# Performance work log

Measured on AMD Instinct MI355X. Metric: run time of the kernel, lower is better.

Reference implementation:

```python
import math
import jax
import jax.numpy as jnp
import numpy as np

B, N = 64, 64
R = N * (N - 1)
DIST_THRESH = 0.35


def _pair_indices(n):
    # edge e = i*(n-1) + j - (j > i): row-major over i, ascending j skipping j == i
    ii = np.repeat(np.arange(n), n - 1)
    jm = np.tile(np.arange(n), (n, 1))
    jj = jm[~np.eye(n, dtype=bool)].reshape(-1)
    return ii, jj


def _rot_basis(a):
    # a: [..., 1] angle -> [..., 2, 2] rotation basis rows [cos,sin],[cos(a+pi/2),sin(a+pi/2)]
    first = jnp.concatenate([jnp.cos(a), jnp.sin(a)], axis=-1)
    second = jnp.concatenate([jnp.cos(a + math.pi / 2), jnp.sin(a + math.pi / 2)], axis=-1)
    return jnp.stack([first, second], axis=-2)


def setup_inputs() -> dict:
    ks = jax.random.split(jax.random.key(0), 8)
    nrm = lambda k, shape, s=1.0: (jax.random.normal(k, shape) * s).astype(jnp.float32)
    return dict(
        objects_state=jax.random.uniform(ks[0], (B, N, 8), dtype=jnp.float32),
        objects_shape=nrm(ks[1], (B, N, 10)),
        relation_info=nrm(ks[2], (B, R, 3)),
        s_mean=jnp.zeros((8,), jnp.float32), s_std=jnp.ones((8,), jnp.float32),
        sh_mean=jnp.zeros((10,), jnp.float32), sh_std=jnp.ones((10,), jnp.float32),
        v_mean=jnp.zeros((3,), jnp.float32), v_std=jnp.ones((3,), jnp.float32),
        W1=nrm(ks[3], (32, 256), 32 ** -0.5), b1=jnp.zeros((256,), jnp.float32),
        W2=nrm(ks[4], (256, 128), 256 ** -0.5), b2=jnp.zeros((128,), jnp.float32),
        W3=nrm(ks[5], (141, 256), 141 ** -0.5), b3=jnp.zeros((256,), jnp.float32),
        W4=nrm(ks[6], (256, 3), 256 ** -0.5), b4=jnp.zeros((3,), jnp.float32),
    )


def reference(objects_state, objects_shape, relation_info, s_mean, s_std, sh_mean, sh_std,
              v_mean, v_std, W1, b1, W2, b2, W3, b3, W4, b4):
    n = objects_state.shape[1]
    ii, jj = _pair_indices(n)

    # ---- pre_proces: distance-threshold edge build into dense one-hot matrices ----
    pos = objects_state[:, :, 0:2]
    dist = jnp.sqrt(jnp.sum((pos[:, :, None, :] - pos[:, None, :, :]) ** 2, axis=-1))
    # torch: where(dist<0.35, dist, 0).nonzero() -> keeps dist<0.35 AND dist != 0 (drops self-edges)
    mask = ((dist < DIST_THRESH) & (dist != 0.0)).astype(jnp.float32)
    mask_flat = mask[:, ii, jj]  # [B, R]
    eye = jnp.eye(n, dtype=jnp.float32)
    receiver_relations = mask_flat[:, :, None] * eye[ii][None]  # [B, R, N]
    sender_relations = mask_flat[:, :, None] * eye[jj][None]    # [B, R, N]

    data_state = (objects_state - s_mean) / s_std
    data_shape = (objects_shape - sh_mean) / sh_std

    senders_state = jnp.einsum('brn,bnd->brd', sender_relations, data_state)
    receivers_state = jnp.einsum('brn,bnd->brd', receiver_relations, data_state)
    senders_shape = jnp.einsum('brn,bnd->brd', sender_relations, data_shape)
    receivers_shape = jnp.einsum('brn,bnd->brd', receiver_relations, data_shape)

    basis = _rot_basis(receivers_state[:, :, 2:3])  # [B, R, 2, 2]
    diff_state = senders_state - receivers_state
    temp = jnp.stack([diff_state[:, :, 0:2], diff_state[:, :, 3:5], senders_state[:, :, 6:8]], axis=-1)  # [B,R,2,3]
    tfed = jnp.einsum('brij,brjk->brik', basis, temp)  # [B,R,2,3]
    angle_diff = diff_state[:, :, 2:3]
    diff_feat = jnp.concatenate([
        tfed[:, :, :, 0], tfed[:, :, :, 1], tfed[:, :, :, 2],
        jnp.sin(2 * angle_diff), jnp.cos(2 * angle_diff),
        diff_state[:, :, 5:6],
    ], axis=-1)  # [B, R, 9]
    rel_data = jnp.concatenate([relation_info, diff_feat, receivers_shape, senders_shape], axis=-1)  # [B,R,32]

    obj_basis = _rot_basis(data_state[:, :, 2:3])  # [B, N, 2, 2]
    obj_vel_tfed = jnp.einsum('bnij,bnj->bni', obj_basis, data_state[:, :, 3:5])
    obj_data = jnp.concatenate([obj_vel_tfed, data_state[:, :, 5:6], data_shape], axis=-1)  # [B,N,13]

    # ---- interaction-network Net ----
    effects = jax.nn.relu(rel_data @ W1 + b1) @ W2 + b2  # [B, R, 128]
    agg = jnp.einsum('brn,bre->bne', receiver_relations, effects)  # [B, N, 128]
    out_vel = jax.nn.relu(jnp.concatenate([obj_data, agg], axis=-1) @ W3 + b3) @ W4 + b4  # [B,N,3]

    # ---- post_proces ----
    angles = objects_state[:, 1:, 2:3]
    pred = out_vel[:, 1:, :] * v_std + v_mean  # inv_transform_vel
    basis_back = _rot_basis(-angles)
    vel_back = jnp.einsum('bnij,bnj->bni', basis_back, pred[:, :, :2])
    x_dot = jnp.concatenate([vel_back, pred[:, :, 2:]], axis=-1)  # [B, N-1, 3]

    tp = np.eye(6, dtype=np.float32)
    tp[3:, 3:] = 0.0
    tq = np.zeros((3, 6), dtype=np.float32)
    for i in range(3):
        tq[i, i] = 1.0
        tq[i, 3 + i] = 1.0
    x_next = objects_state[:, 1:, :6] @ jnp.asarray(tp) + x_dot @ jnp.asarray(tq)
    return x_next  # [B, N-1, 6]
```

## Files before the change

kernel.cpp:

```cpp
#include <hip/hip_runtime.h>
#include <math.h>

#define BB 64
#define NN 64
#define NM1 63
#define RR (NN*(NN-1))

typedef short bf16x8 __attribute__((ext_vector_type(8)));
typedef float f32x4 __attribute__((ext_vector_type(4)));
union U4 { uint4 u; bf16x8 b; };

__device__ inline unsigned int f2bf(float f) {
    unsigned int u = __float_as_uint(f);
    return (u + 0x7FFFu + ((u >> 16) & 1u)) >> 16;
}
__device__ inline unsigned int pack2(float a, float b) {
    return f2bf(a) | (f2bf(b) << 16);
}

__global__ __launch_bounds__(512, 4) void fused_kernel(
    const float* __restrict__ objects_state,
    const float* __restrict__ objects_shape,
    const float* __restrict__ relation_info,
    const float* __restrict__ s_mean, const float* __restrict__ s_std,
    const float* __restrict__ sh_mean, const float* __restrict__ sh_std,
    const float* __restrict__ v_mean, const float* __restrict__ v_std,
    const float* __restrict__ W1, const float* __restrict__ b1,
    const float* __restrict__ W2, const float* __restrict__ b2,
    const float* __restrict__ W3, const float* __restrict__ b3,
    const float* __restrict__ W4, const float* __restrict__ b4,
    float* __restrict__ out)
{
    __shared__ __align__(16) float P[64][28];
    __shared__ __align__(16) unsigned int relb_w[8*64*16];
    __shared__ __align__(16) unsigned short s_h[16*264];
    __shared__ __align__(16) unsigned short s_q[16*168];
    __shared__ int   s_cntg[8];
    __shared__ float s_red[8][16][3];
    __shared__ float s_outv[16][3];

    const int b  = blockIdx.x >> 3;
    const int nb = (blockIdx.x & 7) * 8;
    const int t  = threadIdx.x;
    const int wv = t >> 6, lane = t & 63, col16 = lane & 15, quad = lane >> 4;

    float w1v[16], b10, b11;
    {
        const int cA = wv*32 + col16, cB = cA + 16;
        #pragma unroll
        for (int j = 0; j < 8; ++j) {
            const int k = quad*8 + j;
            const int orig = k < 12 ? k : (k < 22 ? k+10 : k-10);
            w1v[j]   = W1[orig*256 + cA];
            w1v[8+j] = W1[orig*256 + cB];
        }
        b10 = b1[cA]; b11 = b1[cB];
    }

    float ri0 = 0.f, ri1 = 0.f, ri2 = 0.f;
    if (t < 504) {
        const float* rp = relation_info + ((size_t)b*RR + nb*NM1 + t)*3;
        ri0 = rp[0]; ri1 = rp[1]; ri2 = rp[2];
    }

    float e_vs0=0.f,e_vs1=0.f,e_vs2=0.f,e_vm0=0.f,e_vm1=0.f,e_vm2=0.f,e_b4=0.f;
    if (t < 48) {
        e_vs0 = v_std[0]; e_vs1 = v_std[1]; e_vs2 = v_std[2];
        e_vm0 = v_mean[0]; e_vm1 = v_mean[1]; e_vm2 = v_mean[2];
        e_b4  = b4[t % 3];
    }

    {
        uint4 z = make_uint4(0,0,0,0);
        uint4* relb4 = (uint4*)relb_w;
        #pragma unroll
        for (int r = 0; r < 4; ++r) relb4[r*512 + t] = z;
        if (t < 336) ((uint4*)s_q)[t] = z;
        if (t < 8) s_cntg[t] = 0;
        if (t < 64) {
            const int n = b*64 + t;
            const float4* sp4 = (const float4*)(objects_state + (size_t)n*8);
            const float4 sA = sp4[0], sB = sp4[1];
            float st[8] = {sA.x, sA.y, sA.z, sA.w, sB.x, sB.y, sB.z, sB.w};
            const float2* hp2 = (const float2*)(objects_shape + (size_t)n*10);
            float sh[10];
            #pragma unroll
            for (int c = 0; c < 5; ++c) {
                const float2 v = hp2[c];
                sh[c*2] = v.x; sh[c*2+1] = v.y;
            }
            float f[28];
            f[0] = st[0]; f[1] = st[1]; f[26] = st[2]; f[27] = 0.f;
            #pragma unroll
            for (int c = 0; c < 8; ++c)  f[2+c]  = (st[c] - s_mean[c]) / s_std[c];
            #pragma unroll
            for (int c = 0; c < 10; ++c) f[10+c] = (sh[c] - sh_mean[c]) / sh_std[c];
            const float sa = sinf(f[4]), ca = cosf(f[4]);
            const float sr = sinf(st[2]), cr = cosf(st[2]);
            f[20] = ca; f[21] = sa; f[22] = cr; f[23] = sr;
            f[24] =  ca*f[5] + sa*f[6];
            f[25] = -sa*f[5] + ca*f[6];
            float4* dp = (float4*)&P[t][0];
            #pragma unroll
            for (int q = 0; q < 7; ++q)
                dp[q] = make_float4(f[q*4], f[q*4+1], f[q*4+2], f[q*4+3]);
        }
    }
    __syncthreads();

    U4 bu0, bu1;
    bu0.u.x = pack2(w1v[0],  w1v[1]);  bu0.u.y = pack2(w1v[2],  w1v[3]);
    bu0.u.z = pack2(w1v[4],  w1v[5]);  bu0.u.w = pack2(w1v[6],  w1v[7]);
    bu1.u.x = pack2(w1v[8],  w1v[9]);  bu1.u.y = pack2(w1v[10], w1v[11]);
    bu1.u.z = pack2(w1v[12], w1v[13]); bu1.u.w = pack2(w1v[14], w1v[15]);

    if (t < 504) {
        const int g = t/63, k = t - g*63, n = nb + g, j = k + (k >= n);
        const float dx = P[n][0] - P[j][0];
        const float dy = P[n][1] - P[j][1];
        const float dist = sqrtf(dx*dx + dy*dy);
        if (dist < 0.35f && dist != 0.0f) {
            const int slot = atomicAdd(&s_cntg[g], 1);
            const int row = (g << 6) + slot;
            uint4* dst = (uint4*)&relb_w[row*16];
            const float ca = P[n][20], sa = P[n][21];
            const float d0 = P[j][2]-P[n][2], d1 = P[j][3]-P[n][3];
            const float d2 = P[j][4]-P[n][4], d3 = P[j][5]-P[n][5];
            const float d4 = P[j][6]-P[n][6], d5 = P[j][7]-P[n][7];
            uint4 o;
            o.x = pack2(ri0, ri1);
            o.y = pack2(ri2, ca*d0 + sa*d1);
            o.z = pack2(-sa*d0 + ca*d1, ca*d3 + sa*d4);
            o.w = pack2(-sa*d3 + ca*d4, ca*P[j][8] + sa*P[j][9]);
            dst[0] = o;
            o.x = pack2(-sa*P[j][8] + ca*P[j][9], sinf(2.f*d2));
            o.y = pack2(cosf(2.f*d2), d5);
            o.z = pack2(P[j][10], P[j][11]);
            o.w = pack2(P[j][12], P[j][13]);
            dst[1] = o;
            o.x = pack2(P[j][14], P[j][15]);
            o.y = pack2(P[j][16], P[j][17]);
            o.z = pack2(P[j][18], P[j][19]);
            o.w = pack2(P[n][10], P[n][11]);
            dst[2] = o;
            o.x = pack2(P[n][12], P[n][13]);
            o.y = pack2(P[n][14], P[n][15]);
            o.z = pack2(P[n][16], P[n][17]);
            o.w = pack2(P[n][18], P[n][19]);
            dst[3] = o;
        }
    }
    __syncthreads();

    {
        int cg[8];
        #pragma unroll
        for (int g = 0; g < 8; ++g) cg[g] = s_cntg[g];
        float hs0[8], hs1[8];
        #pragma unroll
        for (int g = 0; g < 8; ++g) { hs0[g] = 0.f; hs1[g] = 0.f; }
        #pragma unroll
        for (int g = 0; g < 8; ++g) {
            const int mts = (cg[g] + 15) >> 4;
            for (int mt = 0; mt < mts; ++mt) {
                U4 au;
                au.u = *(const uint4*)&relb_w[((g<<6) + mt*16 + col16)*16 + quad*4];
                f32x4 a0 = {0.f,0.f,0.f,0.f}, a1 = {0.f,0.f,0.f,0.f};
                a0 = __builtin_amdgcn_mfma_f32_16x16x32_bf16(au.b, bu0.b, a0, 0,0,0);
                a1 = __builtin_amdgcn_mfma_f32_16x16x32_bf16(au.b, bu1.b, a1, 0,0,0);
                #pragma unroll
                for (int i = 0; i < 4; ++i) {
                    hs0[g] += fmaxf(a0[i] + b10, 0.f);
                    hs1[g] += fmaxf(a1[i] + b11, 0.f);
                }
            }
        }
        const float rb0 = fmaxf(b10, 0.f), rb1 = fmaxf(b11, 0.f);
        #pragma unroll
        for (int g = 0; g < 8; ++g) {
            const int mts = (cg[g] + 15) >> 4;
            const float pad = (float)(mts*16 - cg[g]);
            float v0 = hs0[g], v1 = hs1[g];
            v0 += __shfl_xor(v0, 16); v0 += __shfl_xor(v0, 32);
            v1 += __shfl_xor(v1, 16); v1 += __shfl_xor(v1, 32);
            if (quad == 0) {
                s_h[g*264 + (wv*2+0)*16 + col16] =
                    (unsigned short)f2bf(v0 - pad*rb0);
                s_h[g*264 + (wv*2+1)*16 + col16] =
                    (unsigned short)f2bf(v1 - pad*rb1);
            }
        }
    }

    U4 w2f[8];
    float b2v;
    {
        #pragma unroll
        for (int kc = 0; kc < 8; ++kc) {
            float v[8];
            #pragma unroll
            for (int j = 0; j < 8; ++j)
                v[j] = W2[(size_t)(kc*32 + quad*8 + j)*128 + wv*16 + col16];
            U4 o;
            o.u.x = pack2(v[0], v[1]); o.u.y = pack2(v[2], v[3]);
            o.u.z = pack2(v[4], v[5]); o.u.w = pack2(v[6], v[7]);
            w2f[kc] = o;
        }
        b2v = b2[wv*16 + col16];
    }
    __syncthreads();

    if (t < 104) {
        const int m = t/13, c = t - m*13, n = nb + m;
        float v;
        if (c == 0) v = P[n][24];
        else if (c == 1) v = P[n][25];
        else if (c == 2) v = P[n][7];
        else v = P[n][10 + c - 3];
        s_q[m*168 + c] = (unsigned short)f2bf(v);
    }
    {
        U4 af[8];
        #pragma unroll
        for (int kc = 0; kc < 8; ++kc)
            af[kc].u = *(const uint4*)&s_h[(lane & 15)*264 + kc*32 + quad*8];
        float cntv[4];
        #pragma unroll
        for (int i = 0; i < 4; ++i)
            cntv[i] = (float)s_cntg[(quad*4 + i) & 7];
        f32x4 acc = {0.f,0.f,0.f,0.f};
        #pragma unroll
        for (int kc = 0; kc < 8; ++kc)
            acc = __builtin_amdgcn_mfma_f32_16x16x32_bf16(af[kc].b, w2f[kc].b, acc, 0,0,0);
        #pragma unroll
        for (int i = 0; i < 4; ++i) {
            const int row = quad*4 + i;
            s_q[row*168 + 13 + wv*16 + col16] =
                (unsigned short)f2bf(acc[i] + cntv[i]*b2v);
        }
    }

    U4 w3f[10];
    float b3p[2], w4p[2][3];
    #pragma unroll
    for (int ntl = 0; ntl < 2; ++ntl) {
        const int col = (wv + ntl*8)*16 + col16;
        b3p[ntl] = b3[col];
        w4p[ntl][0] = W4[col*3+0];
        w4p[ntl][1] = W4[col*3+1];
        w4p[ntl][2] = W4[col*3+2];
        #pragma unroll
        for (int kc = 0; kc < 5; ++kc) {
            float v[8];
            #pragma unroll
            for (int j = 0; j < 8; ++j) {
                const int k = kc*32 + quad*8 + j;
                v[j] = (k < 141) ? W3[(size_t)k*256 + col] : 0.f;
            }
            U4 o;
            o.u.x = pack2(v[0], v[1]); o.u.y = pack2(v[2], v[3]);
            o.u.z = pack2(v[4], v[5]); o.u.w = pack2(v[6], v[7]);
            w3f[ntl*5 + kc] = o;
        }
    }
    __syncthreads();

    {
        U4 af3[5];
        #pragma unroll
        for (int kc = 0; kc < 5; ++kc)
            af3[kc].u = *(const uint4*)&s_q[(lane & 15)*168 + kc*32 + quad*8];
        float p[4][3];
        #pragma unroll
        for (int i = 0; i < 4; ++i) { p[i][0]=0.f; p[i][1]=0.f; p[i][2]=0.f; }
        #pragma unroll
        for (int ntl = 0; ntl < 2; ++ntl) {
            f32x4 acc = {0.f,0.f,0.f,0.f};
            #pragma unroll
            for (int kc = 0; kc < 5; ++kc)
                acc = __builtin_amdgcn_mfma_f32_16x16x32_bf16(
                    af3[kc].b, w3f[ntl*5 + kc].b, acc, 0,0,0);
            const float b3v = b3p[ntl];
            const float w40 = w4p[ntl][0], w41 = w4p[ntl][1], w42 = w4p[ntl][2];
            #pragma unroll
            for (int i = 0; i < 4; ++i) {
                const float h = fmaxf(acc[i] + b3v, 0.f);
                p[i][0] = fmaf(h, w40, p[i][0]);
                p[i][1] = fmaf(h, w41, p[i][1]);
                p[i][2] = fmaf(h, w42, p[i][2]);
            }
        }
        #pragma unroll
        for (int off = 1; off < 16; off <<= 1)
            #pragma unroll
            for (int i = 0; i < 4; ++i) {
                p[i][0] += __shfl_xor(p[i][0], off);
                p[i][1] += __shfl_xor(p[i][1], off);
                p[i][2] += __shfl_xor(p[i][2], off);
            }
        if (col16 == 0)
            #pragma unroll
            for (int i = 0; i < 4; ++i) {
                s_red[wv][quad*4+i][0] = p[i][0];
                s_red[wv][quad*4+i][1] = p[i][1];
                s_red[wv][quad*4+i][2] = p[i][2];
            }
    }
    __syncthreads();
    if (t < 48) {
        const int m = t/3, o = t - m*3;
        float acc = e_b4;
        #pragma unroll
        for (int w = 0; w < 8; ++w) acc += s_red[w][m][o];
        s_outv[m][o] = acc;
    }
    __syncthreads();

    if (t < 48) {
        const int m = t/6, i = t - m*6, n = nb + m;
        if (n >= 1) {
            const float q0 = s_outv[m][0]*e_vs0 + e_vm0;
            const float q1 = s_outv[m][1]*e_vs1 + e_vm1;
            const float q2 = s_outv[m][2]*e_vs2 + e_vm2;
            const float cr = P[n][22], sr = P[n][23];
            const float xd0 = cr*q0 - sr*q1;
            const float xd1 = sr*q0 + cr*q1;
            const int im = i % 3;
            const float xd = (im == 0) ? xd0 : (im == 1) ? xd1 : q2;
            float base = 0.f;
            if (i == 0) base = P[n][0];
            else if (i == 1) base = P[n][1];
            else if (i == 2) base = P[n][26];
            out[((size_t)b*NM1 + (n-1))*6 + i] = base + xd;
        }
    }
}

extern "C" void kernel_launch(void* const* d_in, const int* in_sizes, int n_in,
                              void* d_out, int out_size, void* d_ws, size_t ws_size,
                              hipStream_t stream) {
    const float* objects_state = (const float*)d_in[0];
    const float* objects_shape = (const float*)d_in[1];
    const float* relation_info = (const float*)d_in[2];
    const float* s_mean  = (const float*)d_in[3];
    const float* s_std   = (const float*)d_in[4];
    const float* sh_mean = (const float*)d_in[5];
    const float* sh_std  = (const float*)d_in[6];
    const float* v_mean  = (const float*)d_in[7];
    const float* v_std   = (const float*)d_in[8];
    const float* W1 = (const float*)d_in[9];
    const float* b1 = (const float*)d_in[10];
    const float* W2 = (const float*)d_in[11];
    const float* b2 = (const float*)d_in[12];
    const float* W3 = (const float*)d_in[13];
    const float* b3 = (const float*)d_in[14];
    const float* W4 = (const float*)d_in[15];
    const float* b4 = (const float*)d_in[16];
    (void)d_ws; (void)ws_size; (void)in_sizes; (void)n_in; (void)out_size;

    fused_kernel<<<dim3(BB*8), dim3(512), 0, stream>>>(
        objects_state, objects_shape, relation_info,
        s_mean, s_std, sh_mean, sh_std, v_mean, v_std,
        W1, b1, W2, b2, W3, b3, W4, b4,
        (float*)d_out);
}
```

Measured before the change: 108.7 us.

## Swizzle relation LDS rows, pad P, and interleave weight loads with compute

P is padded to 29 columns and written with scalar stores, which avoids LDS bank conflicts on per-object rows. Relation rows in LDS get an XOR swizzle on their 16-byte chunks so the MFMA A-fragment reads hit fewer conflicting banks. The global loads of W2, W3 and W4 are split into halves and issued earlier, overlapping them with the edge MLP, the aggregation and the first W3 tile. This hides global-load latency behind compute, at the cost of more live registers under launch_bounds(512,4), which could cause spills.

```diff
diff --git a/kernel.cpp b/kernel.cpp
--- a/kernel.cpp
+++ b/kernel.cpp
@@ -31,7 +31,7 @@
     const float* __restrict__ W4, const float* __restrict__ b4,
     float* __restrict__ out)
 {
-    __shared__ __align__(16) float P[64][28];
+    __shared__ __align__(16) float P[64][29];
     __shared__ __align__(16) unsigned int relb_w[8*64*16];
     __shared__ __align__(16) unsigned short s_h[16*264];
     __shared__ __align__(16) unsigned short s_q[16*168];
@@ -100,10 +100,8 @@
             f[20] = ca; f[21] = sa; f[22] = cr; f[23] = sr;
             f[24] =  ca*f[5] + sa*f[6];
             f[25] = -sa*f[5] + ca*f[6];
-            float4* dp = (float4*)&P[t][0];
-            #pragma unroll
-            for (int q = 0; q < 7; ++q)
-                dp[q] = make_float4(f[q*4], f[q*4+1], f[q*4+2], f[q*4+3]);
+            #pragma unroll
+            for (int c = 0; c < 28; ++c) P[t][c] = f[c];
         }
     }
     __syncthreads();
@@ -122,6 +120,7 @@
         if (dist < 0.35f && dist != 0.0f) {
             const int slot = atomicAdd(&s_cntg[g], 1);
             const int row = (g << 6) + slot;
+            const int sw = (row >> 1) & 3;
             uint4* dst = (uint4*)&relb_w[row*16];
             const float ca = P[n][20], sa = P[n][21];
             const float d0 = P[j][2]-P[n][2], d1 = P[j][3]-P[n][3];
@@ -132,26 +131,30 @@
             o.y = pack2(ri2, ca*d0 + sa*d1);
             o.z = pack2(-sa*d0 + ca*d1, ca*d3 + sa*d4);
             o.w = pack2(-sa*d3 + ca*d4, ca*P[j][8] + sa*P[j][9]);
-            dst[0] = o;
+            dst[0 ^ sw] = o;
             o.x = pack2(-sa*P[j][8] + ca*P[j][9], sinf(2.f*d2));
             o.y = pack2(cosf(2.f*d2), d5);
             o.z = pack2(P[j][10], P[j][11]);
             o.w = pack2(P[j][12], P[j][13]);
-            dst[1] = o;
+            dst[1 ^ sw] = o;
             o.x = pack2(P[j][14], P[j][15]);
             o.y = pack2(P[j][16], P[j][17]);
             o.z = pack2(P[j][18], P[j][19]);
             o.w = pack2(P[n][10], P[n][11]);
-            dst[2] = o;
+            dst[2 ^ sw] = o;
             o.x = pack2(P[n][12], P[n][13]);
             o.y = pack2(P[n][14], P[n][15]);
             o.z = pack2(P[n][16], P[n][17]);
             o.w = pack2(P[n][18], P[n][19]);
-            dst[3] = o;
-        }
-    }
-    __syncthreads();
-
+            dst[3 ^ sw] = o;
+        }
+    }
+    __syncthreads();
+
+    const int rd_sw = (quad ^ ((col16 >> 1) & 3)) * 4;
+
+    U4 w2f[8];
+    float b2v;
     {
         int cg[8];
         #pragma unroll
@@ -164,7 +167,7 @@
             const int mts = (cg[g] + 15) >> 4;
             for (int mt = 0; mt < mts; ++mt) {
                 U4 au;
-                au.u = *(const uint4*)&relb_w[((g<<6) + mt*16 + col16)*16 + quad*4];
+                au.u = *(const uint4*)&relb_w[((g<<6) + mt*16 + col16)*16 + rd_sw];
                 f32x4 a0 = {0.f,0.f,0.f,0.f}, a1 = {0.f,0.f,0.f,0.f};
                 a0 = __builtin_amdgcn_mfma_f32_16x16x32_bf16(au.b, bu0.b, a0, 0,0,0);
                 a1 = __builtin_amdgcn_mfma_f32_16x16x32_bf16(au.b, bu1.b, a1, 0,0,0);
@@ -175,6 +178,13 @@
                 }
             }
         }
+        float w2rA[32];
+        #pragma unroll
+        for (int kc = 0; kc < 4; ++kc)
+            #pragma unroll
+            for (int j = 0; j < 8; ++j)
+                w2rA[kc*8+j] = W2[(size_t)(kc*32 + quad*8 + j)*128 + wv*16 + col16];
+        b2v = b2[wv*16 + col16];
         const float rb0 = fmaxf(b10, 0.f), rb1 = fmaxf(b11, 0.f);
         #pragma unroll
         for (int g = 0; g < 8; ++g) {
@@ -190,26 +200,35 @@
                     (unsigned short)f2bf(v1 - pad*rb1);
             }
         }
-    }
-
-    U4 w2f[8];
-    float b2v;
-    {
-        #pragma unroll
-        for (int kc = 0; kc < 8; ++kc) {
-            float v[8];
+        float w2rB[32];
+        #pragma unroll
+        for (int kc = 0; kc < 4; ++kc)
             #pragma unroll
             for (int j = 0; j < 8; ++j)
-                v[j] = W2[(size_t)(kc*32 + quad*8 + j)*128 + wv*16 + col16];
+                w2rB[kc*8+j] = W2[(size_t)((kc+4)*32 + quad*8 + j)*128 + wv*16 + col16];
+        #pragma unroll
+        for (int kc = 0; kc < 4; ++kc) {
             U4 o;
-            o.u.x = pack2(v[0], v[1]); o.u.y = pack2(v[2], v[3]);
-            o.u.z = pack2(v[4], v[5]); o.u.w = pack2(v[6], v[7]);
+            o.u.x = pack2(w2rA[kc*8+0], w2rA[kc*8+1]);
+            o.u.y = pack2(w2rA[kc*8+2], w2rA[kc*8+3]);
+            o.u.z = pack2(w2rA[kc*8+4], w2rA[kc*8+5]);
+            o.u.w = pack2(w2rA[kc*8+6], w2rA[kc*8+7]);
             w2f[kc] = o;
         }
-        b2v = b2[wv*16 + col16];
-    }
-    __syncthreads();
-
+        #pragma unroll
+        for (int kc = 0; kc < 4; ++kc) {
+            U4 o;
+            o.u.x = pack2(w2rB[kc*8+0], w2rB[kc*8+1]);
+            o.u.y = pack2(w2rB[kc*8+2], w2rB[kc*8+3]);
+            o.u.z = pack2(w2rB[kc*8+4], w2rB[kc*8+5]);
+            o.u.w = pack2(w2rB[kc*8+6], w2rB[kc*8+7]);
+            w2f[4+kc] = o;
+        }
+    }
+    __syncthreads();
+
+    U4 w3f0[5];
+    float b3p0, w4p0[3];
     if (t < 104) {
         const int m = t/13, c = t - m*13, n = nb + m;
         float v;
@@ -228,6 +247,19 @@
         #pragma unroll
         for (int i = 0; i < 4; ++i)
             cntv[i] = (float)s_cntg[(quad*4 + i) & 7];
+        float w3r0[40];
+        {
+            const int col = wv*16 + col16;
+            b3p0 = b3[col];
+            w4p0[0] = W4[col*3+0]; w4p0[1] = W4[col*3+1]; w4p0[2] = W4[col*3+2];
+            #pragma unroll
+            for (int kc = 0; kc < 5; ++kc)
+                #pragma unroll
+                for (int j = 0; j < 8; ++j) {
+                    const int k = kc*32 + quad*8 + j;
+                    w3r0[kc*8+j] = (k < 141) ? W3[(size_t)k*256 + col] : 0.f;
+                }
+        }
         f32x4 acc = {0.f,0.f,0.f,0.f};
         #pragma unroll
         for (int kc = 0; kc < 8; ++kc)
@@ -238,29 +270,14 @@
             s_q[row*168 + 13 + wv*16 + col16] =
                 (unsigned short)f2bf(acc[i] + cntv[i]*b2v);
         }
-    }
-
-    U4 w3f[10];
-    float b3p[2], w4p[2][3];
-    #pragma unroll
-    for (int ntl = 0; ntl < 2; ++ntl) {
-        const int col = (wv + ntl*8)*16 + col16;
-        b3p[ntl] = b3[col];
-        w4p[ntl][0] = W4[col*3+0];
-        w4p[ntl][1] = W4[col*3+1];
-        w4p[ntl][2] = W4[col*3+2];
         #pragma unroll
         for (int kc = 0; kc < 5; ++kc) {
-            float v[8];
-            #pragma unroll
-            for (int j = 0; j < 8; ++j) {
-                const int k = kc*32 + quad*8 + j;
-                v[j] = (k < 141) ? W3[(size_t)k*256 + col] : 0.f;
-            }
             U4 o;
-            o.u.x = pack2(v[0], v[1]); o.u.y = pack2(v[2], v[3]);
-            o.u.z = pack2(v[4], v[5]); o.u.w = pack2(v[6], v[7]);
-            w3f[ntl*5 + kc] = o;
+            o.u.x = pack2(w3r0[kc*8+0], w3r0[kc*8+1]);
+            o.u.y = pack2(w3r0[kc*8+2], w3r0[kc*8+3]);
+            o.u.z = pack2(w3r0[kc*8+4], w3r0[kc*8+5]);
+            o.u.w = pack2(w3r0[kc*8+6], w3r0[kc*8+7]);
+            w3f0[kc] = o;
         }
     }
     __syncthreads();
@@ -270,24 +287,58 @@
         #pragma unroll
         for (int kc = 0; kc < 5; ++kc)
             af3[kc].u = *(const uint4*)&s_q[(lane & 15)*168 + kc*32 + quad*8];
+        float w3r1[40], b3p1, w4p1[3];
+        {
+            const int col = (wv + 8)*16 + col16;
+            b3p1 = b3[col];
+            w4p1[0] = W4[col*3+0]; w4p1[1] = W4[col*3+1]; w4p1[2] = W4[col*3+2];
+            #pragma unroll
+            for (int kc = 0; kc < 5; ++kc)
+                #pragma unroll
+                for (int j = 0; j < 8; ++j) {
+                    const int k = kc*32 + quad*8 + j;
+                    w3r1[kc*8+j] = (k < 141) ? W3[(size_t)k*256 + col] : 0.f;
+                }
+        }
         float p[4][3];
         #pragma unroll
         for (int i = 0; i < 4; ++i) { p[i][0]=0.f; p[i][1]=0.f; p[i][2]=0.f; }
-        #pragma unroll
-        for (int ntl = 0; ntl < 2; ++ntl) {
+        {
             f32x4 acc = {0.f,0.f,0.f,0.f};
             #pragma unroll
             for (int kc = 0; kc < 5; ++kc)
                 acc = __builtin_amdgcn_mfma_f32_16x16x32_bf16(
-                    af3[kc].b, w3f[ntl*5 + kc].b, acc, 0,0,0);
-            const float b3v = b3p[ntl];
-            const float w40 = w4p[ntl][0], w41 = w4p[ntl][1], w42 = w4p[ntl][2];
+                    af3[kc].b, w3f0[kc].b, acc, 0,0,0);
             #pragma unroll
             for (int i = 0; i < 4; ++i) {
-                const float h = fmaxf(acc[i] + b3v, 0.f);
-                p[i][0] = fmaf(h, w40, p[i][0]);
-                p[i][1] = fmaf(h, w41, p[i][1]);
-                p[i][2] = fmaf(h, w42, p[i][2]);
+                const float h = fmaxf(acc[i] + b3p0, 0.f);
+                p[i][0] = fmaf(h, w4p0[0], p[i][0]);
+                p[i][1] = fmaf(h, w4p0[1], p[i][1]);
+                p[i][2] = fmaf(h, w4p0[2], p[i][2]);
+            }
+        }
+        {
+            U4 w3f1[5];
+            #pragma unroll
+            for (int kc = 0; kc < 5; ++kc) {
+                U4 o;
+                o.u.x = pack2(w3r1[kc*8+0], w3r1[kc*8+1]);
+                o.u.y = pack2(w3r1[kc*8+2], w3r1[kc*8+3]);
+                o.u.z = pack2(w3r1[kc*8+4], w3r1[kc*8+5]);
+                o.u.w = pack2(w3r1[kc*8+6], w3r1[kc*8+7]);
+                w3f1[kc] = o;
+            }
+            f32x4 acc = {0.f,0.f,0.f,0.f};
+            #pragma unroll
+            for (int kc = 0; kc < 5; ++kc)
+                acc = __builtin_amdgcn_mfma_f32_16x16x32_bf16(
+                    af3[kc].b, w3f1[kc].b, acc, 0,0,0);
+            #pragma unroll
+            for (int i = 0; i < 4; ++i) {
+                const float h = fmaxf(acc[i] + b3p1, 0.f);
+                p[i][0] = fmaf(h, w4p1[0], p[i][0]);
+                p[i][1] = fmaf(h, w4p1[1], p[i][1]);
+                p[i][2] = fmaf(h, w4p1[2], p[i][2]);
             }
         }
         #pragma unroll
```

After: 137.7 us. 1.27x slower.
